# Performance work log

Hardware: AMD Instinct MI355X
Metric: run time of the kernel (lower is better)

Reference implementation:

```python
import jax, jax.numpy as jnp
import numpy as np


def _gcn_conv(x, W, b, src, dst, n):
    # x: [N, F_in] -> project first (dense GEMM), then normalized scatter-add.
    h = x @ W  # [N, F_out]
    deg = jax.ops.segment_sum(jnp.ones_like(dst, dtype=h.dtype), dst, num_segments=n)  # in-degree incl. self loops
    inv_sqrt = jax.lax.rsqrt(deg)  # deg >= 1 because self loops were added
    norm = inv_sqrt[src] * inv_sqrt[dst]  # [E+N]
    out = jax.ops.segment_sum(h[src] * norm[:, None], dst, num_segments=n)  # [N, F_out]
    return out + b


def setup_inputs() -> dict:
    key = jax.random.key(0)
    k1, k2, k3, k4 = jax.random.split(key, 4)
    N, E, F_IN, H, C = 10000, 160000, 3703, 1024, 6
    x = jax.random.normal(k1, (N, F_IN), dtype=jnp.float32)
    edge_index = jax.random.randint(k2, (2, E), 0, N, dtype=jnp.int64)
    # Glorot-style init for weights
    W1 = jax.random.normal(k3, (F_IN, H), dtype=jnp.float32) * np.float32(1.0 / np.sqrt(F_IN))
    W2 = jax.random.normal(k4, (H, C), dtype=jnp.float32) * np.float32(1.0 / np.sqrt(H))
    b1 = jnp.zeros((H,), dtype=jnp.float32)
    b2 = jnp.zeros((C,), dtype=jnp.float32)
    return {"x": x, "edge_index": edge_index, "W1": W1, "b1": b1, "W2": W2, "b2": b2}


def reference(x, edge_index, W1, b1, W2, b2):
    n = x.shape[0]
    # GCNConv adds self loops; degree normalization D^{-1/2}(A+I)D^{-1/2}
    loop = jnp.arange(n, dtype=edge_index.dtype)
    src = jnp.concatenate([edge_index[0], loop])
    dst = jnp.concatenate([edge_index[1], loop])
    h = _gcn_conv(x, W1, b1, src, dst, n)
    h = jax.nn.relu(h)
    # dropout is identity in eval mode
    h = _gcn_conv(h, W2, b2, src, dst, n)
    return jax.nn.log_softmax(h, axis=1)
```

## Files before the change

kernel.cpp:

```cpp
#include <hip/hip_runtime.h>
#include <stdint.h>

typedef unsigned short u16;
typedef unsigned int u32;
typedef __bf16 bf16x8 __attribute__((ext_vector_type(8)));
typedef float f32x4 __attribute__((ext_vector_type(4)));

#define N_NODES 10000
#define N_EDGES 160000
#define F_IN    3703
#define HDIM    1024
#define CDIM    6
#define MP      10112
#define KP      3712
#define KT      58

static __device__ __forceinline__ u16 f2bf(float f) {
    u32 u = __builtin_bit_cast(u32, f);
    u32 r = (u + 0x7fffu + ((u >> 16) & 1u)) >> 16;
    return (u16)r;
}
static __device__ __forceinline__ float bf2f(u16 b) {
    return __builtin_bit_cast(float, ((u32)b) << 16);
}

#define GL2LDS(g, l) __builtin_amdgcn_global_load_lds(                         \
    (const __attribute__((address_space(1))) void*)(g),                        \
    (__attribute__((address_space(3))) void*)(l), 16, 0, 0)

__global__ void k_init(int* counts, int* cursor) {
    int i = blockIdx.x * 256 + threadIdx.x;
    if (i < N_NODES) { counts[i] = 0; cursor[i] = 0; }
}

__global__ void k_count(const int* __restrict__ ei, int* counts) {
    int e = blockIdx.x * 256 + threadIdx.x;
    if (e < N_EDGES) {
        int dst = ei[N_EDGES + e];
        atomicAdd(&counts[dst], 1);
    }
}

__global__ void k_scan(const int* __restrict__ counts, int* __restrict__ offsets,
                       float* __restrict__ inv_sqrt) {
    __shared__ int sums[1024];
    int t = threadIdx.x;
    int local[10];
    int s = 0;
    #pragma unroll
    for (int i = 0; i < 10; i++) {
        int idx = t * 10 + i;
        int v = (idx < N_NODES) ? counts[idx] : 0;
        local[i] = s; s += v;
    }
    sums[t] = s;
    __syncthreads();
    for (int off = 1; off < 1024; off <<= 1) {
        int v = (t >= off) ? sums[t - off] : 0;
        __syncthreads();
        sums[t] += v;
        __syncthreads();
    }
    int base = (t == 0) ? 0 : sums[t - 1];
    #pragma unroll
    for (int i = 0; i < 10; i++) {
        int idx = t * 10 + i;
        if (idx < N_NODES) {
            offsets[idx] = base + local[i];
            inv_sqrt[idx] = rsqrtf((float)(counts[idx] + 1));
        }
    }
    if (t == 1023) offsets[N_NODES] = sums[1023];
}

__global__ void k_fill(const int* __restrict__ ei, const int* __restrict__ offsets,
                       int* cursor, int* __restrict__ edge_src) {
    int e = blockIdx.x * 256 + threadIdx.x;
    if (e < N_EDGES) {
        int src = ei[e];
        int dst = ei[N_EDGES + e];
        int pos = atomicAdd(&cursor[dst], 1);
        edge_src[offsets[dst] + pos] = src;
    }
}

__global__ void k_cvt_x(const float* __restrict__ x, u16* __restrict__ A) {
    const int KP4 = KP / 4;
    int i = blockIdx.x * 256 + threadIdx.x;
    if (i >= MP * KP4) return;
    int m = i / KP4;
    int k4 = (i - m * KP4) * 4;
    float v0 = 0.f, v1 = 0.f, v2 = 0.f, v3 = 0.f;
    if (m < N_NODES) {
        const float* xp = x + (size_t)m * F_IN;
        if (k4 + 3 < F_IN) {
            v0 = xp[k4]; v1 = xp[k4 + 1]; v2 = xp[k4 + 2]; v3 = xp[k4 + 3];
        } else {
            if (k4     < F_IN) v0 = xp[k4];
            if (k4 + 1 < F_IN) v1 = xp[k4 + 1];
            if (k4 + 2 < F_IN) v2 = xp[k4 + 2];
            if (k4 + 3 < F_IN) v3 = xp[k4 + 3];
        }
    }
    ushort4 o;
    o.x = f2bf(v0); o.y = f2bf(v1); o.z = f2bf(v2); o.w = f2bf(v3);
    *(ushort4*)&A[(size_t)m * KP + k4] = o;
}

__global__ void k_cvt_w1t(const float* __restrict__ W1, u16* __restrict__ BT) {
    __shared__ u16 tile[64][66];
    int k0 = blockIdx.x * 64, n0 = blockIdx.y * 64;
    int tx = threadIdx.x & 63, ty = threadIdx.x >> 6;
    #pragma unroll
    for (int i = 0; i < 16; i++) {
        int kk = ty + i * 4;
        int k = k0 + kk;
        float v = (k < F_IN) ? W1[(size_t)k * HDIM + n0 + tx] : 0.f;
        tile[kk][tx] = f2bf(v);
    }
    __syncthreads();
    #pragma unroll
    for (int i = 0; i < 16; i++) {
        int nn = ty + i * 4;
        BT[(size_t)(n0 + nn) * KP + k0 + tx] = tile[tx][nn];
    }
}

__global__ __launch_bounds__(256) void k_gemm1(const u16* __restrict__ A,
                                               const u16* __restrict__ BT,
                                               u16* __restrict__ H1) {
    __shared__ __align__(16) u16 As[128 * 64];
    __shared__ __align__(16) u16 Bs[128 * 64];
    const int tid = threadIdx.x;
    const int lane = tid & 63;
    const int wid = tid >> 6;
    const int wm = wid >> 1, wn = wid & 1;
    const int bn = blockIdx.x, bm = blockIdx.y;

    int srow[4], scol[4], sdst[4];
    #pragma unroll
    for (int j = 0; j < 4; j++) {
        int q = wid * 4 + j;
        int e = q * 512 + lane * 8;
        int row = e >> 6, c = e & 63;
        srow[j] = row;
        scol[j] = c ^ ((row & 7) << 3);
        sdst[j] = q * 512;
    }
    const u16* Abase = A + (size_t)bm * 128 * KP;
    const u16* Bbase = BT + (size_t)bn * 128 * KP;

    f32x4 acc[4][4];
    #pragma unroll
    for (int i = 0; i < 4; i++)
        #pragma unroll
        for (int j = 0; j < 4; j++)
            acc[i][j] = (f32x4)0.f;

    for (int kt = 0; kt < KT; ++kt) {
        const int k0 = kt * 64;
        #pragma unroll
        for (int j = 0; j < 4; j++)
            GL2LDS(Abase + srow[j] * KP + k0 + scol[j], As + sdst[j]);
        #pragma unroll
        for (int j = 0; j < 4; j++)
            GL2LDS(Bbase + srow[j] * KP + k0 + scol[j], Bs + sdst[j]);
        __syncthreads();

        const int rA = wm * 64 + (lane & 15);
        const int rB = wn * 64 + (lane & 15);
        const int cb = (lane >> 4) << 3;
        #pragma unroll
        for (int kk = 0; kk < 2; kk++) {
            bf16x8 av[4], bv[4];
            const int cc = kk * 32 + cb;
            #pragma unroll
            for (int i = 0; i < 4; i++) {
                int r = rA + i * 16;
                av[i] = *(const bf16x8*)(As + r * 64 + (cc ^ ((r & 7) << 3)));
                int r2 = rB + i * 16;
                bv[i] = *(const bf16x8*)(Bs + r2 * 64 + (cc ^ ((r2 & 7) << 3)));
            }
            #pragma unroll
            for (int i = 0; i < 4; i++)
                #pragma unroll
                for (int j = 0; j < 4; j++)
                    acc[i][j] = __builtin_amdgcn_mfma_f32_16x16x32_bf16(
                        av[i], bv[j], acc[i][j], 0, 0, 0);
        }
        __syncthreads();
    }

    const int cr = (lane >> 4) * 4;
    const int ccol = lane & 15;
    #pragma unroll
    for (int i = 0; i < 4; i++) {
        #pragma unroll
        for (int j = 0; j < 4; j++) {
            #pragma unroll
            for (int r = 0; r < 4; r++) {
                int row = bm * 128 + wm * 64 + i * 16 + cr + r;
                if (row < N_NODES) {
                    int col = bn * 128 + wn * 64 + j * 16 + ccol;
                    H1[(size_t)row * HDIM + col] = f2bf(acc[i][j][r]);
                }
            }
        }
    }
}

__global__ void k_agg1(const u16* __restrict__ H1, const int* __restrict__ offsets,
                       const int* __restrict__ edge_src, const float* __restrict__ inv_sqrt,
                       const float* __restrict__ b1, float* __restrict__ AGG1) {
    int node = blockIdx.x;
    int t = threadIdx.x;
    int f = t * 4;
    float is_n = inv_sqrt[node];
    float a0, a1, a2, a3;
    {
        float w = is_n * is_n;
        ushort4 v = *(const ushort4*)(H1 + (size_t)node * HDIM + f);
        a0 = bf2f(v.x) * w; a1 = bf2f(v.y) * w; a2 = bf2f(v.z) * w; a3 = bf2f(v.w) * w;
    }
    int beg = offsets[node], end = offsets[node + 1];
    for (int e = beg; e < end; ++e) {
        int s = edge_src[e];
        float w = inv_sqrt[s] * is_n;
        ushort4 v = *(const ushort4*)(H1 + (size_t)s * HDIM + f);
        a0 += bf2f(v.x) * w; a1 += bf2f(v.y) * w; a2 += bf2f(v.z) * w; a3 += bf2f(v.w) * w;
    }
    float4 o;
    o.x = fmaxf(a0 + b1[f + 0], 0.f);
    o.y = fmaxf(a1 + b1[f + 1], 0.f);
    o.z = fmaxf(a2 + b1[f + 2], 0.f);
    o.w = fmaxf(a3 + b1[f + 3], 0.f);
    *(float4*)&AGG1[(size_t)node * HDIM + f] = o;
}

__global__ void k_gemm2(const float* __restrict__ AGG1, const float* __restrict__ W2,
                        float* __restrict__ H2) {
    __shared__ float w2l[CDIM * HDIM];
    int t = threadIdx.x;
    for (int i = t; i < HDIM * CDIM; i += 256) {
        int k = i / CDIM, c = i - k * CDIM;
        w2l[c * HDIM + k] = W2[i];
    }
    __syncthreads();
    int lane = t & 63, wv = t >> 6;
    int row = blockIdx.x * 4 + wv;
    if (row >= N_NODES) return;
    const float* xp = AGG1 + (size_t)row * HDIM;
    float acc[6] = {0.f, 0.f, 0.f, 0.f, 0.f, 0.f};
    #pragma unroll
    for (int i = 0; i < 16; i++) {
        int k = lane + i * 64;
        float xv = xp[k];
        #pragma unroll
        for (int c = 0; c < 6; c++) acc[c] += xv * w2l[c * HDIM + k];
    }
    #pragma unroll
    for (int c = 0; c < 6; c++) {
        #pragma unroll
        for (int off = 32; off > 0; off >>= 1) acc[c] += __shfl_xor(acc[c], off);
    }
    if (lane == 0) {
        #pragma unroll
        for (int c = 0; c < 6; c++) H2[(size_t)row * CDIM + c] = acc[c];
    }
}

__global__ void k_agg2(const float* __restrict__ H2, const int* __restrict__ offsets,
                       const int* __restrict__ edge_src, const float* __restrict__ inv_sqrt,
                       const float* __restrict__ b2, float* __restrict__ out) {
    int gt = blockIdx.x * 256 + threadIdx.x;
    int node = gt >> 3, sub = gt & 7;
    if (node >= N_NODES) return;
    float is_n = inv_sqrt[node];
    float acc[6] = {0.f, 0.f, 0.f, 0.f, 0.f, 0.f};
    int beg = offsets[node], end = offsets[node + 1];
    for (int e = beg + sub; e < end; e += 8) {
        int s = edge_src[e];
        float w = inv_sqrt[s] * is_n;
        #pragma unroll
        for (int c = 0; c < 6; c++) acc[c] += H2[(size_t)s * CDIM + c] * w;
    }
    if (sub == 0) {
        float w = is_n * is_n;
        #pragma unroll
        for (int c = 0; c < 6; c++) acc[c] += H2[(size_t)node * CDIM + c] * w;
    }
    #pragma unroll
    for (int off = 1; off < 8; off <<= 1) {
        #pragma unroll
        for (int c = 0; c < 6; c++) acc[c] += __shfl_xor(acc[c], off);
    }
    if (sub == 0) {
        float z[6];
        #pragma unroll
        for (int c = 0; c < 6; c++) z[c] = acc[c] + b2[c];
        float m = z[0];
        #pragma unroll
        for (int c = 1; c < 6; c++) m = fmaxf(m, z[c]);
        float ssum = 0.f;
        #pragma unroll
        for (int c = 0; c < 6; c++) ssum += __expf(z[c] - m);
        float l = m + logf(ssum);
        #pragma unroll
        for (int c = 0; c < 6; c++) out[(size_t)node * CDIM + c] = z[c] - l;
    }
}

extern "C" void kernel_launch(void* const* d_in, const int* in_sizes, int n_in,
                              void* d_out, int out_size, void* d_ws, size_t ws_size,
                              hipStream_t stream) {
    const float* x  = (const float*)d_in[0];
    const int*   ei = (const int*)d_in[1];
    const float* W1 = (const float*)d_in[2];
    const float* b1 = (const float*)d_in[3];
    const float* W2 = (const float*)d_in[4];
    const float* b2 = (const float*)d_in[5];
    float* out = (float*)d_out;

    char* ws = (char*)d_ws;
    size_t off = 0;
    auto alloc = [&](size_t bytes) -> void* {
        void* p = ws + off;
        off += (bytes + 255) & ~(size_t)255;
        return p;
    };
    u16* A        = (u16*)alloc((size_t)MP * KP * 2);
    u16* BT       = (u16*)alloc((size_t)HDIM * KP * 2);
    u16* H1       = (u16*)alloc((size_t)N_NODES * HDIM * 2);
    int* counts   = (int*)alloc(N_NODES * 4);
    int* cursor   = (int*)alloc(N_NODES * 4);
    int* offsets  = (int*)alloc((N_NODES + 1) * 4);
    float* inv_sq = (float*)alloc(N_NODES * 4);
    int* edge_src = (int*)alloc(N_EDGES * 4);
    float* AGG1 = (float*)A;
    float* H2   = (float*)BT;

    k_init<<<(N_NODES + 255) / 256, 256, 0, stream>>>(counts, cursor);
    k_count<<<(N_EDGES + 255) / 256, 256, 0, stream>>>(ei, counts);
    k_scan<<<1, 1024, 0, stream>>>(counts, offsets, inv_sq);
    k_fill<<<(N_EDGES + 255) / 256, 256, 0, stream>>>(ei, offsets, cursor, edge_src);

    k_cvt_x<<<(MP * (KP / 4) + 255) / 256, 256, 0, stream>>>(x, A);
    dim3 gT(KP / 64, HDIM / 64);
    k_cvt_w1t<<<gT, 256, 0, stream>>>(W1, BT);

    dim3 gG(HDIM / 128, MP / 128);
    k_gemm1<<<gG, 256, 0, stream>>>(A, BT, H1);

    k_agg1<<<N_NODES, 256, 0, stream>>>(H1, offsets, edge_src, inv_sq, b1, AGG1);
    k_gemm2<<<N_NODES / 4, 256, 0, stream>>>(AGG1, W2, H2);
    k_agg2<<<(N_NODES * 8 + 255) / 256, 256, 0, stream>>>(H2, offsets, edge_src, inv_sq, b2, out);
}
```

Measured before the change: 262.6 us.

## Fuse layer-1 aggregation with layer-2 projection and remap GEMM block order

Merges the first aggregation and the small second GEMM into one kernel: each block applies bias and ReLU, multiplies by W2 in registers, and reduces across warps and lanes, so the 40MB fp32 AGG1 intermediate is never written and read back. The GEMM1 block index is remapped so consecutive workgroups spread across M tiles, which is meant to improve cache locality and balance across XCDs. The init kernel is replaced with memsets. The cost is that W2 is read per thread directly from global memory with a strided pattern, and the partial sums are combined through an extra shared-memory reduction.

```diff
diff --git a/kernel.cpp b/kernel.cpp
--- a/kernel.cpp
+++ b/kernel.cpp
@@ -27,11 +27,6 @@
 #define GL2LDS(g, l) __builtin_amdgcn_global_load_lds(                         \
     (const __attribute__((address_space(1))) void*)(g),                        \
     (__attribute__((address_space(3))) void*)(l), 16, 0, 0)
-
-__global__ void k_init(int* counts, int* cursor) {
-    int i = blockIdx.x * 256 + threadIdx.x;
-    if (i < N_NODES) { counts[i] = 0; cursor[i] = 0; }
-}
 
 __global__ void k_count(const int* __restrict__ ei, int* counts) {
     int e = blockIdx.x * 256 + threadIdx.x;
@@ -135,7 +130,11 @@
     const int lane = tid & 63;
     const int wid = tid >> 6;
     const int wm = wid >> 1, wn = wid & 1;
-    const int bn = blockIdx.x, bm = blockIdx.y;
+
+    const u32 orig = (u32)blockIdx.y * 8u + (u32)blockIdx.x;
+    const u32 lin  = (orig & 7u) * 79u + (orig >> 3);
+    const int bm = (int)(lin >> 3);
+    const int bn = (int)(lin & 7u);
 
     int srow[4], scol[4], sdst[4];
     #pragma unroll
@@ -209,9 +208,11 @@
     }
 }
 
-__global__ void k_agg1(const u16* __restrict__ H1, const int* __restrict__ offsets,
-                       const int* __restrict__ edge_src, const float* __restrict__ inv_sqrt,
-                       const float* __restrict__ b1, float* __restrict__ AGG1) {
+__global__ void k_agg1g2(const u16* __restrict__ H1, const int* __restrict__ offsets,
+                         const int* __restrict__ edge_src, const float* __restrict__ inv_sqrt,
+                         const float* __restrict__ b1, const float* __restrict__ W2,
+                         float* __restrict__ H2) {
+    __shared__ float red[4][8];
     int node = blockIdx.x;
     int t = threadIdx.x;
     int f = t * 4;
@@ -229,43 +230,30 @@
         ushort4 v = *(const ushort4*)(H1 + (size_t)s * HDIM + f);
         a0 += bf2f(v.x) * w; a1 += bf2f(v.y) * w; a2 += bf2f(v.z) * w; a3 += bf2f(v.w) * w;
     }
-    float4 o;
-    o.x = fmaxf(a0 + b1[f + 0], 0.f);
-    o.y = fmaxf(a1 + b1[f + 1], 0.f);
-    o.z = fmaxf(a2 + b1[f + 2], 0.f);
-    o.w = fmaxf(a3 + b1[f + 3], 0.f);
-    *(float4*)&AGG1[(size_t)node * HDIM + f] = o;
-}
-
-__global__ void k_gemm2(const float* __restrict__ AGG1, const float* __restrict__ W2,
-                        float* __restrict__ H2) {
-    __shared__ float w2l[CDIM * HDIM];
-    int t = threadIdx.x;
-    for (int i = t; i < HDIM * CDIM; i += 256) {
-        int k = i / CDIM, c = i - k * CDIM;
-        w2l[c * HDIM + k] = W2[i];
+    float4 bb = *(const float4*)(b1 + f);
+    float z0 = fmaxf(a0 + bb.x, 0.f);
+    float z1 = fmaxf(a1 + bb.y, 0.f);
+    float z2 = fmaxf(a2 + bb.z, 0.f);
+    float z3 = fmaxf(a3 + bb.w, 0.f);
+    float acc[6];
+    #pragma unroll
+    for (int c = 0; c < 6; c++)
+        acc[c] = z0 * W2[(size_t)f * 6 + c] + z1 * W2[(size_t)(f + 1) * 6 + c]
+               + z2 * W2[(size_t)(f + 2) * 6 + c] + z3 * W2[(size_t)(f + 3) * 6 + c];
+    #pragma unroll
+    for (int c = 0; c < 6; c++) {
+        #pragma unroll
+        for (int off = 32; off > 0; off >>= 1) acc[c] += __shfl_xor(acc[c], off);
+    }
+    int lane = t & 63, wv = t >> 6;
+    if (lane == 0) {
+        #pragma unroll
+        for (int c = 0; c < 6; c++) red[wv][c] = acc[c];
     }
     __syncthreads();
-    int lane = t & 63, wv = t >> 6;
-    int row = blockIdx.x * 4 + wv;
-    if (row >= N_NODES) return;
-    const float* xp = AGG1 + (size_t)row * HDIM;
-    float acc[6] = {0.f, 0.f, 0.f, 0.f, 0.f, 0.f};
-    #pragma unroll
-    for (int i = 0; i < 16; i++) {
-        int k = lane + i * 64;
-        float xv = xp[k];
-        #pragma unroll
-        for (int c = 0; c < 6; c++) acc[c] += xv * w2l[c * HDIM + k];
-    }
-    #pragma unroll
-    for (int c = 0; c < 6; c++) {
-        #pragma unroll
-        for (int off = 32; off > 0; off >>= 1) acc[c] += __shfl_xor(acc[c], off);
-    }
-    if (lane == 0) {
-        #pragma unroll
-        for (int c = 0; c < 6; c++) H2[(size_t)row * CDIM + c] = acc[c];
+    if (t < 6) {
+        float s = red[0][t] + red[1][t] + red[2][t] + red[3][t];
+        H2[(size_t)node * CDIM + t] = s;
     }
 }
 
@@ -336,10 +324,10 @@
     int* offsets  = (int*)alloc((N_NODES + 1) * 4);
     float* inv_sq = (float*)alloc(N_NODES * 4);
     int* edge_src = (int*)alloc(N_EDGES * 4);
-    float* AGG1 = (float*)A;
-    float* H2   = (float*)BT;
-
-    k_init<<<(N_NODES + 255) / 256, 256, 0, stream>>>(counts, cursor);
+    float* H2 = (float*)BT;
+
+    hipMemsetAsync(counts, 0, N_NODES * 4, stream);
+    hipMemsetAsync(cursor, 0, N_NODES * 4, stream);
     k_count<<<(N_EDGES + 255) / 256, 256, 0, stream>>>(ei, counts);
     k_scan<<<1, 1024, 0, stream>>>(counts, offsets, inv_sq);
     k_fill<<<(N_EDGES + 255) / 256, 256, 0, stream>>>(ei, offsets, cursor, edge_src);
@@ -351,7 +339,6 @@
     dim3 gG(HDIM / 128, MP / 128);
     k_gemm1<<<gG, 256, 0, stream>>>(A, BT, H1);
 
-    k_agg1<<<N_NODES, 256, 0, stream>>>(H1, offsets, edge_src, inv_sq, b1, AGG1);
-    k_gemm2<<<N_NODES / 4, 256, 0, stream>>>(AGG1, W2, H2);
+    k_agg1g2<<<N_NODES, 256, 0, stream>>>(H1, offsets, edge_src, inv_sq, b1, W2, H2);
     k_agg2<<<(N_NODES * 8 + 255) / 256, 256, 0, stream>>>(H2, offsets, edge_src, inv_sq, b2, out);
 }
```

Result: faster. 240.1 us (-8.6%).
